# Kernel tuning notes

Measured on AMD Instinct MI355X. Metric: run time of the kernel, lower is better.

Reference implementation:

```python
import jax, jax.numpy as jnp
import numpy as np

ALPHA = 2.0  # spikingjelly default ATan surrogate alpha
EPS = 1e-5   # BatchNorm eps

@jax.custom_vjp
def heaviside_atan(x):
    return (x >= 0.0).astype(x.dtype)

def _ha_fwd(x):
    return heaviside_atan(x), x

def _ha_bwd(x, g):
    return (g * ALPHA / (2.0 * (1.0 + (jnp.pi / 2.0 * ALPHA * x) ** 2)),)

heaviside_atan.defvjp(_ha_fwd, _ha_bwd)

def lif(x_seq, tau=2.0, v_th=1.0):
    # MultiStepLIFNode, v_reset=0 (hard reset), detach_reset=True
    def step(v, x):
        v = v + (x - v) / tau
        s = heaviside_atan(v - v_th)
        v = v * (1.0 - jax.lax.stop_gradient(s))
        return v, s
    _, spikes = jax.lax.scan(step, jnp.zeros_like(x_seq[0]), x_seq)
    return spikes

def conv_bn(y, Wt, g, b):
    # 1x1 conv (no bias) + BatchNorm2d in training mode over flattened (T*B, H, W)
    y = jnp.einsum('tbchw,oc->tbohw', y, Wt)
    m = y.mean(axis=(0, 1, 3, 4), keepdims=True)
    v = y.var(axis=(0, 1, 3, 4), keepdims=True)
    C = Wt.shape[0]
    return (y - m) / jnp.sqrt(v + EPS) * g.reshape(1, 1, C, 1, 1) + b.reshape(1, 1, C, 1, 1)

def setup_inputs() -> dict:
    key = jax.random.key(0)
    ks = jax.random.split(key, 5)
    T, B, C, H, W = 4, 64, 384, 14, 14
    x = jax.random.normal(ks[0], (T, B, C, H, W), dtype=jnp.float32)
    Wq = jax.random.normal(ks[1], (C, C), dtype=jnp.float32) * 0.02
    Wk = jax.random.normal(ks[2], (C, C), dtype=jnp.float32) * 0.02
    Wv = jax.random.normal(ks[3], (C, C), dtype=jnp.float32) * 0.02
    Wp = jax.random.normal(ks[4], (C, C), dtype=jnp.float32) * 0.02
    ones = jnp.ones((C,), jnp.float32)
    zeros = jnp.zeros((C,), jnp.float32)
    return {"x": x, "Wq": Wq, "Wk": Wk, "Wv": Wv, "Wp": Wp,
            "gq": ones, "bq": zeros, "gk": ones, "bk": zeros,
            "gv": ones, "bv": zeros, "gp": ones, "bp": zeros}

def reference(x, Wq, Wk, Wv, Wp, gq, bq, gk, bk, gv, bv, gp, bp):
    T, B, C, H, W = x.shape
    nh = 8
    dh = C // nh
    N = H * W

    xs = lif(x)  # pre_lif

    def heads(y):  # [T,B,C,H,W] -> [T,B,h,N,dh]
        y = y.reshape(T, B, C, N).transpose(0, 1, 3, 2)
        return y.reshape(T, B, N, nh, dh).transpose(0, 1, 3, 2, 4)

    q = heads(lif(conv_bn(xs, Wq, gq, bq)))
    k = heads(lif(conv_bn(xs, Wk, gk, bk)))
    v = heads(lif(conv_bn(xs, Wv, gv, bv)))

    attn = jnp.einsum('tbhnd,tbhmd->tbhnm', q, k)      # no softmax
    o = jnp.einsum('tbhnm,tbhmd->tbhnd', attn, v) * 0.125
    o = o.transpose(0, 1, 2, 4, 3).reshape(T, B, C, N).reshape(T, B, C, H, W)
    o = lif(o, v_th=0.5)                                # attn_lif
    return conv_bn(o, Wp, gp, bp)                       # proj (no lif)
```

## Files before the change

### kernel.cpp

```cpp
#include <hip/hip_runtime.h>
#include <hip/hip_bf16.h>
#include <stdint.h>

#define T_  4
#define B_  64
#define C_  384
#define N_  196
#define NH  8
#define DH  48
#define TB_ (T_*B_)
#define R_  (T_*B_*N_)
#define NW  12
#define P_  12544
#define NCH 66
#define KG_ 17

typedef float f32x2 __attribute__((ext_vector_type(2)));

__global__ void transpose_w4(const float* __restrict__ s0, const float* __restrict__ s1,
                             const float* __restrict__ s2, const float* __restrict__ s3,
                             float* __restrict__ dst){
    int m = blockIdx.y;
    const float* src = (m==0)?s0:(m==1)?s1:(m==2)?s2:s3;
    int idx = blockIdx.x*256 + threadIdx.x;
    if (idx >= C_*C_) return;
    int o = idx % C_, c = idx / C_;
    dst[(size_t)m*C_*C_ + idx] = src[o*C_ + c];
}

__global__ __launch_bounds__(256) void pre_lif(const float* __restrict__ x,
                                               uint32_t* __restrict__ maskXS){
    int b = blockIdx.x / NW;
    int w = blockIdx.x % NW;
    int n = threadIdx.x;
    if (n >= N_) return;
    float v[32];
#pragma unroll
    for (int j=0;j<32;j++) v[j] = 0.f;
#pragma unroll
    for (int t=0;t<T_;t++){
        uint32_t word = 0;
#pragma unroll
        for (int j=0;j<32;j++){
            int c = w*32 + j;
            float xv = x[((size_t)(t*B_+b)*C_ + c)*N_ + n];
            v[j] = v[j] + (xv - v[j])*0.5f;
            if (v[j] >= 1.0f){ word |= (1u<<j); v[j] = 0.f; }
        }
        maskXS[((size_t)(t*B_+b)*N_ + n)*NW + w] = word;
    }
}

__global__ __launch_bounds__(256) void bit_transpose(const uint32_t* __restrict__ mask,
                                                     unsigned long long* __restrict__ maskT){
    int gw = blockIdx.x*4 + (threadIdx.x>>6);
    int lane = threadIdx.x & 63;
    int kc = gw/12, kw = gw%12;
    uint32_t mwv[12];
#pragma unroll
    for (int w=0;w<12;w++) mwv[w]=0u;
    if (gw < 784){
        int pix = gw*64 + lane;
        const uint4* m4 = (const uint4*)(mask + (size_t)pix*NW);
        uint4 a=m4[0], b=m4[1], c=m4[2];
        mwv[0]=a.x; mwv[1]=a.y; mwv[2]=a.z; mwv[3]=a.w;
        mwv[4]=b.x; mwv[5]=b.y; mwv[6]=b.z; mwv[7]=b.w;
        mwv[8]=c.x; mwv[9]=c.y; mwv[10]=c.z; mwv[11]=c.w;
    }
#pragma unroll
    for (int w=0; w<12; w++){
        uint32_t word = mwv[w];
#pragma unroll
        for (int j=0; j<32; j++){
            unsigned long long bal = __ballot((int)((word>>j)&1u));
            if (lane == 0)
                maskT[((size_t)kc*C_ + (w*32+j))*12 + kw] = bal;
        }
    }
}

__global__ __launch_bounds__(256) void gram(const unsigned long long* __restrict__ maskT,
                                            unsigned int* __restrict__ Gpart){
    __shared__ unsigned int tile[64][49];
    int tid = threadIdx.x, wave = tid>>6, lane = tid&63;
    int kg = blockIdx.x, rg = blockIdx.y, cg = blockIdx.z;
    for (int i=tid; i<64*49; i+=256) ((unsigned int*)tile)[i] = 0u;
    __syncthreads();
    int kc = kg*4 + wave;
    if (kc < NCH){
        const uint4* rp = (const uint4*)(maskT + ((size_t)kc*C_ + rg*64 + lane)*12);
        uint32_t row[24];
#pragma unroll
        for (int q=0;q<6;q++){
            uint4 a = rp[q];
            row[4*q]=a.x; row[4*q+1]=a.y; row[4*q+2]=a.z; row[4*q+3]=a.w;
        }
        for (int cc=0; cc<48; cc++){
            const uint4* cp = (const uint4*)(maskT + ((size_t)kc*C_ + cg*48 + cc)*12);
            uint32_t col[24];
#pragma unroll
            for (int q=0;q<6;q++){
                uint4 a = cp[q];
                col[4*q]=a.x; col[4*q+1]=a.y; col[4*q+2]=a.z; col[4*q+3]=a.w;
            }
            unsigned int s = 0;
#pragma unroll
            for (int q=0;q<24;q++) s += (unsigned int)__popc(row[q]&col[q]);
            atomicAdd(&tile[lane][cc], s);
        }
    }
    __syncthreads();
    unsigned int* out = Gpart + (size_t)kg*C_*C_;
    for (int i=tid; i<64*48; i+=256){
        int r = i/48, cc = i%48;
        out[(size_t)(rg*64+r)*C_ + cg*48 + cc] = tile[r][cc];
    }
}

__global__ __launch_bounds__(256) void gram_reduce(const unsigned int* __restrict__ Gpart,
                                                   float* __restrict__ Gf){
    int e = blockIdx.x*256 + threadIdx.x;
    unsigned int s = 0;
#pragma unroll
    for (int k=0;k<KG_;k++) s += Gpart[(size_t)k*C_*C_ + e];
    Gf[e] = (float)s;
}

__global__ __launch_bounds__(384) void bn_from_gram(const float* __restrict__ Gf,
        const float* __restrict__ WTall,
        const float* __restrict__ g0, const float* __restrict__ b0,
        const float* __restrict__ g1, const float* __restrict__ b1,
        const float* __restrict__ g2, const float* __restrict__ b2,
        float* __restrict__ scaleOut, float* __restrict__ shiftOut, int wtBase){
    __shared__ float w4[384][4];
    __shared__ float sred[8][6];
    int t = threadIdx.x, wave = t>>6, lane = t&63;
    int br = blockIdx.y;
    const float* WT = WTall + (size_t)(wtBase+br)*C_*C_;
    int o0 = blockIdx.x*4;
    float4 wv = *(const float4*)(WT + (size_t)t*C_ + o0);
    w4[t][0]=wv.x; w4[t][1]=wv.y; w4[t][2]=wv.z; w4[t][3]=wv.w;
    __syncthreads();
    float h0=0.f,h1=0.f,h2=0.f,h3=0.f;
#pragma unroll 4
    for (int c=0;c<C_;c++){
        float gv = Gf[(size_t)c*C_ + t];
        float4 wc = *(const float4*)&w4[c][0];
        h0 += gv*wc.x; h1 += gv*wc.y; h2 += gv*wc.z; h3 += gv*wc.w;
    }
    float cnt = Gf[(size_t)t*C_ + t];
    float p0=wv.x*h0, p1=wv.y*h1, p2=wv.z*h2, p3=wv.w*h3;
    float q0=cnt*wv.x, q1=cnt*wv.y, q2=cnt*wv.z, q3=cnt*wv.w;
#pragma unroll
    for (int off=32; off>0; off>>=1){
        p0+=__shfl_down(p0,off); p1+=__shfl_down(p1,off);
        p2+=__shfl_down(p2,off); p3+=__shfl_down(p3,off);
        q0+=__shfl_down(q0,off); q1+=__shfl_down(q1,off);
        q2+=__shfl_down(q2,off); q3+=__shfl_down(q3,off);
    }
    if (lane == 0){
        sred[0][wave]=p0; sred[1][wave]=p1; sred[2][wave]=p2; sred[3][wave]=p3;
        sred[4][wave]=q0; sred[5][wave]=q1; sred[6][wave]=q2; sred[7][wave]=q3;
    }
    __syncthreads();
    if (t < 4){
        const float* g  = (br==0)?g0:(br==1)?g1:g2;
        const float* bb = (br==0)?b0:(br==1)?b1:b2;
        float ss = ((sred[t][0]+sred[t][1])+(sred[t][2]+sred[t][3]))+(sred[t][4]+sred[t][5]);
        float sm = ((sred[4+t][0]+sred[4+t][1])+(sred[4+t][2]+sred[4+t][3]))+(sred[4+t][4]+sred[4+t][5]);
        float m   = sm / (float)R_;
        float var = ss / (float)R_ - m*m;
        float sc  = g[o0+t] / sqrtf(var + 1e-5f);
        scaleOut[br*C_ + o0+t] = sc;
        shiftOut[br*C_ + o0+t] = bb[o0+t] - m*sc;
    }
}

__global__ __launch_bounds__(256) void conv_lif(const uint32_t* __restrict__ mask,
                                                const float* __restrict__ WTall,
                                                const float* __restrict__ scaleAll,
                                                const float* __restrict__ shiftAll,
                                                uint32_t* __restrict__ moQ,
                                                uint32_t* __restrict__ moK,
                                                uint32_t* __restrict__ moV){
    __shared__ uint16_t lst[4][400];
    int br = blockIdx.y;
    const float* WT = WTall + (size_t)br*C_*C_;
    uint32_t* mo = (br==0)?moQ:(br==1)?moK:moV;
    int tid = threadIdx.x, wave = tid>>6, lane = tid&63;
    int pix0 = blockIdx.x*4 + wave;
    float sc[6], sh[6], v[6];
#pragma unroll
    for (int i=0;i<6;i++){
        sc[i] = scaleAll[br*C_ + (i<<6) + lane];
        sh[i] = shiftAll[br*C_ + (i<<6) + lane];
        v[i]  = 0.f;
    }
    for (int t=0;t<T_;t++){
        size_t pix = (size_t)t*P_ + pix0;
        const uint4* m4 = (const uint4*)(mask + pix*NW);
        uint4 ma = m4[0], mb = m4[1], mc = m4[2];
        uint32_t mwv[12] = {ma.x,ma.y,ma.z,ma.w, mb.x,mb.y,mb.z,mb.w, mc.x,mc.y,mc.z,mc.w};
        int cnt = 0;
#pragma unroll
        for (int w=0;w<12;w++) cnt += __popc(mwv[w]);
        if (lane == 0){
            int k = 0;
#pragma unroll
            for (int w=0;w<12;w++){
                uint32_t bits = mwv[w];
                while (bits){
                    lst[wave][k++] = (uint16_t)((w<<5) + __builtin_ctz(bits));
                    bits &= bits - 1;
                }
            }
        }
        float ya[6]={0,0,0,0,0,0}, yb[6]={0,0,0,0,0,0};
        float yc[6]={0,0,0,0,0,0}, yd[6]={0,0,0,0,0,0};
        int i = 0;
        for (; i+3 < cnt; i += 4){
            ushort4 cs = *(const ushort4*)&lst[wave][i];
            const float* q0 = WT + (size_t)cs.x*C_ + lane;
            const float* q1 = WT + (size_t)cs.y*C_ + lane;
            const float* q2 = WT + (size_t)cs.z*C_ + lane;
            const float* q3 = WT + (size_t)cs.w*C_ + lane;
#pragma unroll
            for (int j=0;j<6;j++){
                ya[j] += q0[j<<6]; yb[j] += q1[j<<6];
                yc[j] += q2[j<<6]; yd[j] += q3[j<<6];
            }
        }
        for (; i < cnt; ++i){
            int c = lst[wave][i];
            const float* q0 = WT + (size_t)c*C_ + lane;
#pragma unroll
            for (int j=0;j<6;j++) ya[j] += q0[j<<6];
        }
        uint32_t words[12];
#pragma unroll
        for (int j=0;j<6;j++){
            float val = ((ya[j]+yb[j]) + (yc[j]+yd[j]))*sc[j] + sh[j];
            v[j] = v[j] + (val - v[j])*0.5f;
            int s = (v[j] >= 1.0f);
            unsigned long long bal = __ballot(s);
            if (s) v[j] = 0.f;
            words[2*j]   = (uint32_t)bal;
            words[2*j+1] = (uint32_t)(bal>>32);
        }
        if (lane == 0){
            uint4* o4 = (uint4*)(mo + pix*NW);
            o4[0] = make_uint4(words[0],words[1],words[2],words[3]);
            o4[1] = make_uint4(words[4],words[5],words[6],words[7]);
            o4[2] = make_uint4(words[8],words[9],words[10],words[11]);
        }
    }
}

__global__ __launch_bounds__(256) void attention_lif(const uint32_t* __restrict__ mq,
                                                     const uint32_t* __restrict__ mk,
                                                     const uint32_t* __restrict__ mv,
                                                     uint16_t* __restrict__ mo){
    __shared__ unsigned long long kT[DH][4];
    __shared__ unsigned long long vT[DH][4];
    __shared__ uint32_t Cp[DH*25];

    int h = blockIdx.x & 7;
    int b = blockIdx.x >> 3;
    int tid = threadIdx.x, wv = tid>>6, lane = tid&63;
    int sw  = (h*DH) >> 5;
    int shf = (h*DH) & 31;

    float vm[DH];
#pragma unroll
    for (int d=0;d<DH;d++) vm[d] = 0.f;

    for (int t=0;t<T_;t++){
        int tb = t*B_ + b;
        unsigned long long q = 0, kk = 0, vvv = 0;
        if (tid < N_){
            const uint32_t* pq = mq + ((size_t)tb*N_ + tid)*NW + sw;
            const uint32_t* pk = mk + ((size_t)tb*N_ + tid)*NW + sw;
            const uint32_t* pv = mv + ((size_t)tb*N_ + tid)*NW + sw;
            unsigned long long lo, hi;
            lo = pq[0]; hi = pq[1];
            q   = (shf ? ((lo>>16) | (hi<<16)) : (lo | (hi<<32))) & 0xFFFFFFFFFFFFULL;
            lo = pk[0]; hi = pk[1];
            kk  = (shf ? ((lo>>16) | (hi<<16)) : (lo | (hi<<32))) & 0xFFFFFFFFFFFFULL;
            lo = pv[0]; hi = pv[1];
            vvv = (shf ? ((lo>>16) | (hi<<16)) : (lo | (hi<<32))) & 0xFFFFFFFFFFFFULL;
        }
#pragma unroll 1
        for (int d=0; d<DH; d++){
            unsigned long long bk_ = __ballot((int)((kk >>d)&1ull));
            unsigned long long bv_ = __ballot((int)((vvv>>d)&1ull));
            if (lane == 0){ kT[d][wv] = bk_; vT[d][wv] = bv_; }
        }
        __syncthreads();

        if (tid < 240){
            int j  = tid / 5;
            int dg = tid % 5;
            int d0 = dg*10;
            int d1 = (dg==4) ? 48 : d0+10;
            unsigned long long ka=kT[j][0], kb=kT[j][1], kc=kT[j][2], kd=kT[j][3];
            for (int d=d0; d<d1; d+=2){
                uint32_t c0 = (uint32_t)(__popcll(ka&vT[d][0]) + __popcll(kb&vT[d][1])
                            + __popcll(kc&vT[d][2]) + __popcll(kd&vT[d][3]));
                uint32_t c1 = (uint32_t)(__popcll(ka&vT[d+1][0]) + __popcll(kb&vT[d+1][1])
                            + __popcll(kc&vT[d+1][2]) + __popcll(kd&vT[d+1][3]));
                Cp[j*25 + (d>>1)] = c0 | (c1<<16);
            }
        }
        __syncthreads();

        if (tid < N_){
            uint32_t acc[24];
#pragma unroll
            for (int p=0;p<24;p++) acc[p] = 0u;
            unsigned long long qb = q;
            while (qb){
                int j = __builtin_ctzll(qb); qb &= qb-1;
                const uint32_t* row = &Cp[j*25];
#pragma unroll
                for (int p=0;p<24;p++) acc[p] += row[p];
            }
            unsigned long long sp = 0;
#pragma unroll
            for (int d=0; d<DH; d++){
                uint32_t a = (d&1) ? (acc[d>>1]>>16) : (acc[d>>1]&0xFFFFu);
                float o = 0.125f*(float)a;
                vm[d] = vm[d] + (o - vm[d])*0.5f;
                if (vm[d] >= 0.5f){ sp |= (1ull<<d); vm[d] = 0.f; }
            }
            size_t rec = ((size_t)tb*N_ + tid)*24 + 3*h;
            mo[rec]   = (uint16_t)(sp);
            mo[rec+1] = (uint16_t)(sp >> 16);
            mo[rec+2] = (uint16_t)(sp >> 32);
        }
        __syncthreads();
    }
}

__global__ __launch_bounds__(256) void proj_out(const uint32_t* __restrict__ mask,
                                                const float* __restrict__ WT,
                                                const float* __restrict__ scale,
                                                const float* __restrict__ shift,
                                                float* __restrict__ out){
    __shared__ float tile[192][98];
    __shared__ uint16_t lst[4][400];
    int bid = blockIdx.x;
    int tb = bid>>2, nh = (bid>>1)&1, ch = bid&1;
    int n0 = nh*98, c0 = ch*192;
    int tid = threadIdx.x, wave = tid>>6, lane = tid&63;
    float sc[3], sh[3];
#pragma unroll
    for (int i=0;i<3;i++){
        sc[i] = scale[c0+(i<<6)+lane];
        sh[i] = shift[c0+(i<<6)+lane];
    }
    for (int p=wave; p<98; p+=4){
        size_t pix = (size_t)tb*N_ + n0 + p;
        const uint4* m4 = (const uint4*)(mask + pix*NW);
        uint4 ma = m4[0], mb = m4[1], mc = m4[2];
        uint32_t mwv[12] = {ma.x,ma.y,ma.z,ma.w, mb.x,mb.y,mb.z,mb.w, mc.x,mc.y,mc.z,mc.w};
        int cnt = 0;
#pragma unroll
        for (int w=0;w<12;w++) cnt += __popc(mwv[w]);
        if (lane == 0){
            int k = 0;
#pragma unroll
            for (int w=0;w<12;w++){
                uint32_t bits = mwv[w];
                while (bits){
                    lst[wave][k++] = (uint16_t)((w<<5) + __builtin_ctz(bits));
                    bits &= bits - 1;
                }
            }
        }
        float ya[3]={0,0,0}, yb[3]={0,0,0}, yc[3]={0,0,0}, yd[3]={0,0,0};
        int i = 0;
        for (; i+3 < cnt; i += 4){
            ushort4 cs = *(const ushort4*)&lst[wave][i];
            const float* q0 = WT + (size_t)cs.x*C_ + c0 + lane;
            const float* q1 = WT + (size_t)cs.y*C_ + c0 + lane;
            const float* q2 = WT + (size_t)cs.z*C_ + c0 + lane;
            const float* q3 = WT + (size_t)cs.w*C_ + c0 + lane;
#pragma unroll
            for (int j=0;j<3;j++){
                ya[j] += q0[j<<6]; yb[j] += q1[j<<6];
                yc[j] += q2[j<<6]; yd[j] += q3[j<<6];
            }
        }
        for (; i < cnt; ++i){
            int c = lst[wave][i];
            const float* q0 = WT + (size_t)c*C_ + c0 + lane;
#pragma unroll
            for (int j=0;j<3;j++) ya[j] += q0[j<<6];
        }
#pragma unroll
        for (int j=0;j<3;j++)
            tile[(j<<6)+lane][p] = ((ya[j]+yb[j])+(yc[j]+yd[j]))*sc[j] + sh[j];
    }
    __syncthreads();
    for (int r=wave; r<192; r+=4){
        if (lane < 49){
            f32x2 tv = *(const f32x2*)&tile[r][2*lane];
            *(f32x2*)(out + ((size_t)tb*C_ + c0 + r)*N_ + n0 + 2*lane) = tv;
        }
    }
}

extern "C" void kernel_launch(void* const* d_in, const int* in_sizes, int n_in,
                              void* d_out, int out_size, void* d_ws, size_t ws_size,
                              hipStream_t stream) {
    const float* x  = (const float*)d_in[0];
    const float* Wq = (const float*)d_in[1];
    const float* Wk = (const float*)d_in[2];
    const float* Wv = (const float*)d_in[3];
    const float* Wp = (const float*)d_in[4];
    const float* gq = (const float*)d_in[5];
    const float* bq = (const float*)d_in[6];
    const float* gk = (const float*)d_in[7];
    const float* bk = (const float*)d_in[8];
    const float* gv = (const float*)d_in[9];
    const float* bv = (const float*)d_in[10];
    const float* gp = (const float*)d_in[11];
    const float* bp = (const float*)d_in[12];

    char* w = (char*)d_ws;
    size_t off = 0;
    uint32_t* maskXS = (uint32_t*)(w + off); off += (size_t)R_*NW*4;
    uint32_t* maskQ  = (uint32_t*)(w + off); off += (size_t)R_*NW*4;
    uint32_t* maskK  = (uint32_t*)(w + off); off += (size_t)R_*NW*4;
    uint32_t* maskV  = (uint32_t*)(w + off); off += (size_t)R_*NW*4;
    float* WTall = (float*)(w + off); off += (size_t)4*C_*C_*4;
    unsigned long long* maskT = (unsigned long long*)(w + off); off += (size_t)NCH*C_*12*8;
    unsigned int* Gpart = (unsigned int*)(w + off); off += (size_t)KG_*C_*C_*4;
    float* Gf = (float*)(w + off); off += (size_t)C_*C_*4;
    float* scaleB = (float*)(w + off); off += (size_t)4*C_*4;
    float* shiftB = (float*)(w + off); off += (size_t)4*C_*4;
    uint32_t* maskOL = maskXS;

    transpose_w4<<<dim3((C_*C_+255)/256, 4),256,0,stream>>>(Wq, Wk, Wv, Wp, WTall);

    pre_lif<<<B_*NW,256,0,stream>>>(x, maskXS);

    bit_transpose<<<198,256,0,stream>>>(maskXS, maskT);
    gram<<<dim3(KG_,6,8),256,0,stream>>>(maskT, Gpart);
    gram_reduce<<<576,256,0,stream>>>(Gpart, Gf);
    bn_from_gram<<<dim3(96,3),384,0,stream>>>(Gf, WTall, gq,bq, gk,bk, gv,bv,
                                              scaleB, shiftB, 0);

    conv_lif<<<dim3(P_/4,3),256,0,stream>>>(maskXS, WTall, scaleB, shiftB,
                                            maskQ, maskK, maskV);

    attention_lif<<<B_*NH,256,0,stream>>>(maskQ, maskK, maskV, (uint16_t*)maskOL);

    bit_transpose<<<198,256,0,stream>>>(maskOL, maskT);
    gram<<<dim3(KG_,6,8),256,0,stream>>>(maskT, Gpart);
    gram_reduce<<<576,256,0,stream>>>(Gpart, Gf);
    bn_from_gram<<<dim3(96,1),384,0,stream>>>(Gf, WTall, gp,bp, gp,bp, gp,bp,
                                              scaleB + 3*C_, shiftB + 3*C_, 3);

    proj_out<<<TB_*4,256,0,stream>>>(maskOL, WTall + (size_t)3*C_*C_,
                                     scaleB + 3*C_, shiftB + 3*C_, (float*)d_out);
}
```

Before: 422.6 us.

## Stage weight chunks in LDS and tile sixteen pixels per conv_lif block

```diff
diff --git a/kernel.cpp b/kernel.cpp
--- a/kernel.cpp
+++ b/kernel.cpp
@@ -14,6 +14,7 @@
 #define P_  12544
 #define NCH 66
 #define KG_ 17
+#define PIX 16
 
 typedef float f32x2 __attribute__((ext_vector_type(2)));
 
@@ -176,82 +177,96 @@
     }
 }
 
-__global__ __launch_bounds__(256) void conv_lif(const uint32_t* __restrict__ mask,
-                                                const float* __restrict__ WTall,
-                                                const float* __restrict__ scaleAll,
-                                                const float* __restrict__ shiftAll,
-                                                uint32_t* __restrict__ moQ,
-                                                uint32_t* __restrict__ moK,
-                                                uint32_t* __restrict__ moV){
-    __shared__ uint16_t lst[4][400];
-    int br = blockIdx.y;
-    const float* WT = WTall + (size_t)br*C_*C_;
-    uint32_t* mo = (br==0)?moQ:(br==1)?moK:moV;
+__global__ __launch_bounds__(256, 4) void conv_lif_t(const uint32_t* __restrict__ mask,
+        const float* __restrict__ WTall,
+        const float* __restrict__ scaleAll, const float* __restrict__ shiftAll,
+        uint32_t* __restrict__ moQ, uint32_t* __restrict__ moK, uint32_t* __restrict__ moV){
+    __shared__ float wchunk[32*C_];
+    __shared__ uint32_t lm[PIX][4][12];
     int tid = threadIdx.x, wave = tid>>6, lane = tid&63;
-    int pix0 = blockIdx.x*4 + wave;
-    float sc[6], sh[6], v[6];
-#pragma unroll
-    for (int i=0;i<6;i++){
-        sc[i] = scaleAll[br*C_ + (i<<6) + lane];
-        sh[i] = shiftAll[br*C_ + (i<<6) + lane];
-        v[i]  = 0.f;
-    }
-    for (int t=0;t<T_;t++){
-        size_t pix = (size_t)t*P_ + pix0;
-        const uint4* m4 = (const uint4*)(mask + pix*NW);
-        uint4 ma = m4[0], mb = m4[1], mc = m4[2];
-        uint32_t mwv[12] = {ma.x,ma.y,ma.z,ma.w, mb.x,mb.y,mb.z,mb.w, mc.x,mc.y,mc.z,mc.w};
-        int cnt = 0;
-#pragma unroll
-        for (int w=0;w<12;w++) cnt += __popc(mwv[w]);
-        if (lane == 0){
-            int k = 0;
-#pragma unroll
-            for (int w=0;w<12;w++){
-                uint32_t bits = mwv[w];
-                while (bits){
-                    lst[wave][k++] = (uint16_t)((w<<5) + __builtin_ctz(bits));
-                    bits &= bits - 1;
+    int pix0 = blockIdx.x*PIX;
+
+    for (int i = tid; i < PIX*4*12; i += 256){
+        int t = i / (PIX*12), r = i % (PIX*12);
+        int p = r / 12, w = r % 12;
+        lm[p][t][w] = mask[((size_t)t*P_ + pix0 + p)*NW + w];
+    }
+
+    int pbase = wave*4;
+    for (int br = 0; br < 3; ++br){
+        float y[4][4][6];
+#pragma unroll
+        for (int p=0;p<4;p++)
+#pragma unroll
+            for (int tt=0;tt<4;tt++)
+#pragma unroll
+                for (int j=0;j<6;j++) y[p][tt][j] = 0.f;
+
+        const float* WT = WTall + (size_t)br*C_*C_;
+        for (int ch = 0; ch < 12; ++ch){
+            __syncthreads();
+            const float4* src = (const float4*)(WT + (size_t)ch*32*C_);
+            float4* dst = (float4*)wchunk;
+#pragma unroll
+            for (int k = 0; k < 12; ++k)
+                dst[tid + k*256] = src[tid + k*256];
+            __syncthreads();
+#pragma unroll
+            for (int p = 0; p < 4; ++p){
+#pragma unroll
+                for (int tt = 0; tt < 4; ++tt){
+                    uint32_t bits = lm[pbase+p][tt][ch];
+                    while (bits){
+                        int c = __builtin_ctz(bits); bits &= bits - 1;
+                        const float* col = wchunk + c*C_ + lane*6;
+                        f32x2 a = *(const f32x2*)(col);
+                        f32x2 b = *(const f32x2*)(col+2);
+                        f32x2 d = *(const f32x2*)(col+4);
+                        y[p][tt][0] += a.x; y[p][tt][1] += a.y;
+                        y[p][tt][2] += b.x; y[p][tt][3] += b.y;
+                        y[p][tt][4] += d.x; y[p][tt][5] += d.y;
+                    }
                 }
             }
         }
-        float ya[6]={0,0,0,0,0,0}, yb[6]={0,0,0,0,0,0};
-        float yc[6]={0,0,0,0,0,0}, yd[6]={0,0,0,0,0,0};
-        int i = 0;
-        for (; i+3 < cnt; i += 4){
-            ushort4 cs = *(const ushort4*)&lst[wave][i];
-            const float* q0 = WT + (size_t)cs.x*C_ + lane;
-            const float* q1 = WT + (size_t)cs.y*C_ + lane;
-            const float* q2 = WT + (size_t)cs.z*C_ + lane;
-            const float* q3 = WT + (size_t)cs.w*C_ + lane;
-#pragma unroll
-            for (int j=0;j<6;j++){
-                ya[j] += q0[j<<6]; yb[j] += q1[j<<6];
-                yc[j] += q2[j<<6]; yd[j] += q3[j<<6];
-            }
-        }
-        for (; i < cnt; ++i){
-            int c = lst[wave][i];
-            const float* q0 = WT + (size_t)c*C_ + lane;
-#pragma unroll
-            for (int j=0;j<6;j++) ya[j] += q0[j<<6];
-        }
-        uint32_t words[12];
-#pragma unroll
-        for (int j=0;j<6;j++){
-            float val = ((ya[j]+yb[j]) + (yc[j]+yd[j]))*sc[j] + sh[j];
-            v[j] = v[j] + (val - v[j])*0.5f;
-            int s = (v[j] >= 1.0f);
-            unsigned long long bal = __ballot(s);
-            if (s) v[j] = 0.f;
-            words[2*j]   = (uint32_t)bal;
-            words[2*j+1] = (uint32_t)(bal>>32);
-        }
-        if (lane == 0){
-            uint4* o4 = (uint4*)(mo + pix*NW);
-            o4[0] = make_uint4(words[0],words[1],words[2],words[3]);
-            o4[1] = make_uint4(words[4],words[5],words[6],words[7]);
-            o4[2] = make_uint4(words[8],words[9],words[10],words[11]);
+        __syncthreads();
+        uint32_t* mypack = ((uint32_t*)wchunk) + wave*192;
+        for (int i = lane; i < 192; i += 64) mypack[i] = 0u;
+        __syncthreads();
+
+        int o0 = lane*6, w0 = o0 >> 5, shf = o0 & 31;
+#pragma unroll
+        for (int p = 0; p < 4; ++p){
+            float vv[6] = {0.f,0.f,0.f,0.f,0.f,0.f};
+#pragma unroll
+            for (int tt = 0; tt < 4; ++tt){
+                uint32_t bits6 = 0;
+#pragma unroll
+                for (int j = 0; j < 6; ++j){
+                    float sc = scaleAll[br*C_ + o0 + j];
+                    float sh = shiftAll[br*C_ + o0 + j];
+                    float val = y[p][tt][j]*sc + sh;
+                    vv[j] = vv[j] + (val - vv[j])*0.5f;
+                    if (vv[j] >= 1.0f){ bits6 |= (1u<<j); vv[j] = 0.f; }
+                }
+                int inst = p*4 + tt;
+                atomicOr(&mypack[inst*12 + w0], bits6 << shf);
+                if (shf > 26)
+                    atomicOr(&mypack[inst*12 + w0 + 1], bits6 >> (32-shf));
+            }
+        }
+        __syncthreads();
+        uint32_t* mo = (br==0)?moQ:(br==1)?moK:moV;
+        if (lane < 48){
+            int inst = lane >> 2;
+            int q = lane % 3;
+        }
+        if (lane < 48){
+            int inst = lane / 3, q = lane % 3;
+            int p = inst >> 2, tt = inst & 3;
+            uint4 val = *(const uint4*)&mypack[inst*12 + q*4];
+            size_t g = ((size_t)tt*P_ + pix0 + pbase + p)*NW + q*4;
+            *(uint4*)(mo + g) = val;
         }
     }
 }
@@ -451,8 +466,8 @@
     bn_from_gram<<<dim3(96,3),384,0,stream>>>(Gf, WTall, gq,bq, gk,bk, gv,bv,
                                               scaleB, shiftB, 0);
 
-    conv_lif<<<dim3(P_/4,3),256,0,stream>>>(maskXS, WTall, scaleB, shiftB,
-                                            maskQ, maskK, maskV);
+    conv_lif_t<<<P_/PIX,256,0,stream>>>(maskXS, WTall, scaleB, shiftB,
+                                        maskQ, maskK, maskV);
 
     attention_lif<<<B_*NH,256,0,stream>>>(maskQ, maskK, maskV, (uint16_t*)maskOL);
 
```

Result: slower. 555.0 us (+31.3%).

## Fuse Q/K/V spike-conv branches into one kernel sharing the spike index list

Applied to the files above, without the earlier changes.

```diff
diff --git a/kernel.cpp b/kernel.cpp
--- a/kernel.cpp
+++ b/kernel.cpp
@@ -176,26 +176,19 @@
     }
 }
 
-__global__ __launch_bounds__(256) void conv_lif(const uint32_t* __restrict__ mask,
-                                                const float* __restrict__ WTall,
-                                                const float* __restrict__ scaleAll,
-                                                const float* __restrict__ shiftAll,
-                                                uint32_t* __restrict__ moQ,
-                                                uint32_t* __restrict__ moK,
-                                                uint32_t* __restrict__ moV){
-    __shared__ uint16_t lst[4][400];
-    int br = blockIdx.y;
-    const float* WT = WTall + (size_t)br*C_*C_;
-    uint32_t* mo = (br==0)?moQ:(br==1)?moK:moV;
+__global__ __launch_bounds__(256) void conv_lif3(const uint32_t* __restrict__ mask,
+        const float* __restrict__ WTall,
+        const float* __restrict__ scaleAll, const float* __restrict__ shiftAll,
+        uint32_t* __restrict__ moQ, uint32_t* __restrict__ moK, uint32_t* __restrict__ moV){
+    __shared__ uint16_t lst[4][416];
+    __shared__ float scLDS[3*C_];
+    __shared__ float shLDS[3*C_];
     int tid = threadIdx.x, wave = tid>>6, lane = tid&63;
     int pix0 = blockIdx.x*4 + wave;
-    float sc[6], sh[6], v[6];
-#pragma unroll
-    for (int i=0;i<6;i++){
-        sc[i] = scaleAll[br*C_ + (i<<6) + lane];
-        sh[i] = shiftAll[br*C_ + (i<<6) + lane];
-        v[i]  = 0.f;
-    }
+    for (int i=tid; i<3*C_; i+=256){ scLDS[i]=scaleAll[i]; shLDS[i]=shiftAll[i]; }
+    __syncthreads();
+
+    float v0[6]={0,0,0,0,0,0}, v1[6]={0,0,0,0,0,0}, v2[6]={0,0,0,0,0,0};
     for (int t=0;t<T_;t++){
         size_t pix = (size_t)t*P_ + pix0;
         const uint4* m4 = (const uint4*)(mask + pix*NW);
@@ -204,55 +197,69 @@
         int cnt = 0;
 #pragma unroll
         for (int w=0;w<12;w++) cnt += __popc(mwv[w]);
-        if (lane == 0){
-            int k = 0;
+        if (lane < 12){
+            int off = 0;
+            uint32_t mybits = 0;
 #pragma unroll
             for (int w=0;w<12;w++){
-                uint32_t bits = mwv[w];
-                while (bits){
-                    lst[wave][k++] = (uint16_t)((w<<5) + __builtin_ctz(bits));
-                    bits &= bits - 1;
+                if (w < lane) off += __popc(mwv[w]);
+                if (w == lane) mybits = mwv[w];
+            }
+            while (mybits){
+                lst[wave][off++] = (uint16_t)((lane<<5) + __builtin_ctz(mybits));
+                mybits &= mybits - 1;
+            }
+        }
+        __syncthreads();
+
+#pragma unroll
+        for (int br=0; br<3; ++br){
+            const float* WT = WTall + (size_t)br*C_*C_ + lane;
+            float ya[6]={0,0,0,0,0,0}, yb[6]={0,0,0,0,0,0};
+            float yc[6]={0,0,0,0,0,0}, yd[6]={0,0,0,0,0,0};
+            int i = 0;
+            for (; i+3 < cnt; i += 4){
+                ushort4 cs = *(const ushort4*)&lst[wave][i];
+                const float* q0 = WT + (size_t)cs.x*C_;
+                const float* q1 = WT + (size_t)cs.y*C_;
+                const float* q2 = WT + (size_t)cs.z*C_;
+                const float* q3 = WT + (size_t)cs.w*C_;
+#pragma unroll
+                for (int j=0;j<6;j++){
+                    ya[j] += q0[j<<6]; yb[j] += q1[j<<6];
+                    yc[j] += q2[j<<6]; yd[j] += q3[j<<6];
                 }
             }
-        }
-        float ya[6]={0,0,0,0,0,0}, yb[6]={0,0,0,0,0,0};
-        float yc[6]={0,0,0,0,0,0}, yd[6]={0,0,0,0,0,0};
-        int i = 0;
-        for (; i+3 < cnt; i += 4){
-            ushort4 cs = *(const ushort4*)&lst[wave][i];
-            const float* q0 = WT + (size_t)cs.x*C_ + lane;
-            const float* q1 = WT + (size_t)cs.y*C_ + lane;
-            const float* q2 = WT + (size_t)cs.z*C_ + lane;
-            const float* q3 = WT + (size_t)cs.w*C_ + lane;
+            for (; i < cnt; ++i){
+                int c = lst[wave][i];
+                const float* q0 = WT + (size_t)c*C_;
+#pragma unroll
+                for (int j=0;j<6;j++) ya[j] += q0[j<<6];
+            }
+            float* vs = (br==0)?v0:(br==1)?v1:v2;
+            uint32_t words[12];
 #pragma unroll
             for (int j=0;j<6;j++){
-                ya[j] += q0[j<<6]; yb[j] += q1[j<<6];
-                yc[j] += q2[j<<6]; yd[j] += q3[j<<6];
-            }
-        }
-        for (; i < cnt; ++i){
-            int c = lst[wave][i];
-            const float* q0 = WT + (size_t)c*C_ + lane;
-#pragma unroll
-            for (int j=0;j<6;j++) ya[j] += q0[j<<6];
-        }
-        uint32_t words[12];
-#pragma unroll
-        for (int j=0;j<6;j++){
-            float val = ((ya[j]+yb[j]) + (yc[j]+yd[j]))*sc[j] + sh[j];
-            v[j] = v[j] + (val - v[j])*0.5f;
-            int s = (v[j] >= 1.0f);
-            unsigned long long bal = __ballot(s);
-            if (s) v[j] = 0.f;
-            words[2*j]   = (uint32_t)bal;
-            words[2*j+1] = (uint32_t)(bal>>32);
-        }
-        if (lane == 0){
-            uint4* o4 = (uint4*)(mo + pix*NW);
-            o4[0] = make_uint4(words[0],words[1],words[2],words[3]);
-            o4[1] = make_uint4(words[4],words[5],words[6],words[7]);
-            o4[2] = make_uint4(words[8],words[9],words[10],words[11]);
-        }
+                int o = (j<<6) + lane;
+                float val = ((ya[j]+yb[j])+(yc[j]+yd[j]))*scLDS[br*C_+o] + shLDS[br*C_+o];
+                float vv = vs[j];
+                vv = vv + (val - vv)*0.5f;
+                int s = (vv >= 1.0f);
+                unsigned long long bal = __ballot(s);
+                if (s) vv = 0.f;
+                vs[j] = vv;
+                words[2*j]   = (uint32_t)bal;
+                words[2*j+1] = (uint32_t)(bal>>32);
+            }
+            if (lane == 0){
+                uint32_t* mo = (br==0)?moQ:(br==1)?moK:moV;
+                uint4* o4 = (uint4*)(mo + pix*NW);
+                o4[0] = make_uint4(words[0],words[1],words[2],words[3]);
+                o4[1] = make_uint4(words[4],words[5],words[6],words[7]);
+                o4[2] = make_uint4(words[8],words[9],words[10],words[11]);
+            }
+        }
+        __syncthreads();
     }
 }
 
@@ -451,8 +458,8 @@
     bn_from_gram<<<dim3(96,3),384,0,stream>>>(Gf, WTall, gq,bq, gk,bk, gv,bv,
                                               scaleB, shiftB, 0);
 
-    conv_lif<<<dim3(P_/4,3),256,0,stream>>>(maskXS, WTall, scaleB, shiftB,
-                                            maskQ, maskK, maskV);
+    conv_lif3<<<P_/4,256,0,stream>>>(maskXS, WTall, scaleB, shiftB,
+                                     maskQ, maskK, maskV);
 
     attention_lif<<<B_*NH,256,0,stream>>>(maskQ, maskK, maskV, (uint16_t*)maskOL);
 
```

New measurement: 418.9 us. About the same (-0.9%).
